# Kernel optimization log

Measured on AMD Instinct MI355X. Metric: run time of the kernel, lower is better.

Reference implementation:

```python
import math
import jax, jax.numpy as jnp
import numpy as np

NUM_HEAD = 16

def get_slopes(n):
    def pow2(n):
        start = 2 ** (-(2 ** (-(math.log2(n) - 3))))
        return [start * start ** i for i in range(n)]
    if math.log2(n).is_integer():
        return pow2(n)
    c = 2 ** math.floor(math.log2(n))
    return pow2(c) + get_slopes(2 * c)[0::2][: n - c]

def setup_inputs() -> dict:
    key = jax.random.key(0)
    ks = jax.random.split(key, 5)
    B, T, D = 2, 2048, 1024
    x = jax.random.normal(ks[0], (B, T, D), dtype=jnp.float32)
    Wq = jax.random.normal(ks[1], (D, D), dtype=jnp.float32) * 0.02
    Wk = jax.random.normal(ks[2], (D, D), dtype=jnp.float32) * 0.02
    Wv = jax.random.normal(ks[3], (D, D), dtype=jnp.float32) * 0.02
    Wo = jax.random.normal(ks[4], (D, D), dtype=jnp.float32) * (0.02 / math.sqrt(2 * 24))
    return {"x": x, "Wq": Wq, "Wk": Wk, "Wv": Wv, "Wo": Wo}

def reference(x, Wq, Wk, Wv, Wo):
    B, T, D = x.shape
    H = NUM_HEAD
    hd = D // H
    # projections (no bias)
    q = (x @ Wq).reshape(B, T, H, hd).transpose(0, 2, 1, 3)  # b h t d
    k = (x @ Wk).reshape(B, T, H, hd).transpose(0, 2, 1, 3)
    v = (x @ Wv).reshape(B, T, H, hd).transpose(0, 2, 1, 3)
    scores = jnp.einsum("bhqd,bhkd->bhqk", q, k) / jnp.sqrt(jnp.asarray(hd, dtype=q.dtype))
    # ALiBi bias: slopes[h] * (j - (T-1)), broadcast over query positions
    slopes = jnp.asarray(np.array(get_slopes(H), dtype=np.float32))
    alibi = slopes[:, None, None] * (jnp.arange(T, dtype=jnp.float32) - (T - 1))[None, None, :]  # h 1 k
    scores = scores + alibi[None]  # b h q k
    causal = jnp.tril(jnp.ones((T, T), dtype=bool))
    masked = jnp.where(causal[None, None], scores.astype(jnp.float32), jnp.finfo(jnp.float32).min)
    p = jax.nn.softmax(masked, axis=-1)
    attn_out = jnp.einsum("bhqk,bhkd->bhqd", p, v)
    attn_out = attn_out.transpose(0, 2, 1, 3).reshape(B, T, D)
    return attn_out @ Wo
```

## Files before the change

kernel.cpp:

```cpp
#include <hip/hip_runtime.h>
#include <hip/hip_bf16.h>
#include <math.h>

#define B_ 2
#define T_ 2048
#define D_ 1024
#define H_ 16
#define HD 64

typedef __bf16 bf16;
typedef bf16 bf16x8 __attribute__((ext_vector_type(8)));
typedef bf16 bf16x4 __attribute__((ext_vector_type(4)));
typedef short short4v __attribute__((ext_vector_type(4)));
typedef float f32x4 __attribute__((ext_vector_type(4)));

#define GL2LDS16(g, l) __builtin_amdgcn_global_load_lds(                      \
    (const __attribute__((address_space(1))) void*)(g),                       \
    (__attribute__((address_space(3))) void*)(l), 16, 0, 0)

static __device__ __forceinline__ f32x4 mfma16x16x16(bf16x4 a, bf16x4 b, f32x4 c) {
#if defined(__HIP_DEVICE_COMPILE__)
# if __has_builtin(__builtin_amdgcn_mfma_f32_16x16x16bf16_1k)
    return __builtin_amdgcn_mfma_f32_16x16x16bf16_1k(
        __builtin_bit_cast(short4v, a), __builtin_bit_cast(short4v, b), c, 0, 0, 0);
# else
    asm("v_mfma_f32_16x16x16_bf16 %0, %1, %2, %0" : "+v"(c) : "v"(a), "v"(b));
    return c;
# endif
#else
    (void)a; (void)b;
    return c;
#endif
}

static __device__ __forceinline__ bf16x4 lo4(bf16x8 v) {
    return __builtin_shufflevector(v, v, 0, 1, 2, 3);
}
static __device__ __forceinline__ bf16x4 hi4(bf16x8 v) {
    return __builtin_shufflevector(v, v, 4, 5, 6, 7);
}

__global__ __launch_bounds__(256) void prep_inputs(const float* __restrict__ x,
                                                   const float* __restrict__ W0,
                                                   const float* __restrict__ W1,
                                                   const float* __restrict__ W2,
                                                   const float* __restrict__ W3,
                                                   bf16* __restrict__ xb,
                                                   bf16* __restrict__ Wt) {
    const int z = blockIdx.z;
    const int tid = threadIdx.x;
    if (z >= 4) {
        size_t i = ((((size_t)(z - 4) * 256 + blockIdx.y * 16 + blockIdx.x) * 256) + tid) * 4;
        float4 v = *(const float4*)(x + i);
        bf16 tmp[4] = {(bf16)v.x, (bf16)v.y, (bf16)v.z, (bf16)v.w};
        *(uint2*)(xb + i) = *(const uint2*)tmp;
        return;
    }
    __shared__ bf16 tile[64 * 72];
    const float* W = (z == 0) ? W0 : (z == 1) ? W1 : (z == 2) ? W2 : W3;
    bf16* out = Wt + (size_t)z * D_ * D_;
    const int k0 = blockIdx.y * 64, n0 = blockIdx.x * 64;
    for (int it = 0; it < 4; ++it) {
        int idx = it * 256 + tid;
        int r = idx >> 4;
        int c4 = (idx & 15) << 2;
        float4 v = *(const float4*)(W + (size_t)(k0 + r) * D_ + n0 + c4);
        tile[(c4 + 0) * 72 + r] = (bf16)v.x;
        tile[(c4 + 1) * 72 + r] = (bf16)v.y;
        tile[(c4 + 2) * 72 + r] = (bf16)v.z;
        tile[(c4 + 3) * 72 + r] = (bf16)v.w;
    }
    __syncthreads();
    for (int it = 0; it < 2; ++it) {
        int idx = it * 256 + tid;
        int r = idx >> 3;
        int c8 = (idx & 7) << 3;
        bf16x8 v = *(const bf16x8*)&tile[r * 72 + c8];
        *(bf16x8*)(out + (size_t)(n0 + r) * D_ + k0 + c8) = v;
    }
}

__global__ __launch_bounds__(256) void gemm_qkv(const bf16* __restrict__ A,
                                                const bf16* __restrict__ Bt,
                                                bf16* __restrict__ Cout) {
    __shared__ bf16 As[2][128 * 32];
    __shared__ bf16 Bs[2][64 * 32];
    const int bid = blockIdx.x;
    const int xcd = bid & 7, rr = bid >> 3;
    const int y   = (xcd << 2) + (rr & 3);
    const int rem = rr >> 2;
    const int xx  = rem & 15;
    const int z   = rem >> 4;
    const int m0 = y * 128, n0 = xx * 64;

    const int tid = threadIdx.x;
    const int wave = tid >> 6, lane = tid & 63;
    const int quad = lane >> 4, l16 = lane & 15;
    const int wr = wave >> 1, wc = wave & 1;
    const bf16* Bz = Bt + (size_t)z * D_ * D_;

    const int lrow = lane >> 2, lcol = (lane & 3) << 3;
    const bf16* ag = A  + (size_t)(m0 + wave * 32 + lrow) * D_ + lcol;
    const bf16* bg = Bz + (size_t)(n0 + wave * 16 + lrow) * D_ + lcol;
    const int a_off = (wave * 32 + lrow) * 32 + lcol;
    const int b_off = (wave * 16 + lrow) * 32 + lcol;

    f32x4 acc[4][2];
    for (int mi = 0; mi < 4; ++mi)
        for (int ni = 0; ni < 2; ++ni) acc[mi][ni] = (f32x4){0.f, 0.f, 0.f, 0.f};

    for (int kb = 0; kb < D_; kb += 64) {
        GL2LDS16(ag + kb,                        &As[0][a_off]);
        GL2LDS16(ag + (size_t)16 * D_ + kb,      &As[0][a_off + 16 * 32]);
        GL2LDS16(ag + kb + 32,                   &As[1][a_off]);
        GL2LDS16(ag + (size_t)16 * D_ + kb + 32, &As[1][a_off + 16 * 32]);
        GL2LDS16(bg + kb,                        &Bs[0][b_off]);
        GL2LDS16(bg + kb + 32,                   &Bs[1][b_off]);
        __syncthreads();

        for (int half = 0; half < 2; ++half) {
            bf16x8 af[4], bfr[2];
            for (int mi = 0; mi < 4; ++mi)
                af[mi] = *(const bf16x8*)&As[half][(wr * 64 + mi * 16 + l16) * 32 + quad * 8];
            for (int ni = 0; ni < 2; ++ni)
                bfr[ni] = *(const bf16x8*)&Bs[half][(wc * 32 + ni * 16 + l16) * 32 + quad * 8];
            if (z < 2) {
                for (int mi = 0; mi < 4; ++mi)
                    for (int ni = 0; ni < 2; ++ni)
                        acc[mi][ni] = __builtin_amdgcn_mfma_f32_16x16x32_bf16(
                            bfr[ni], af[mi], acc[mi][ni], 0, 0, 0);
            } else {
                for (int mi = 0; mi < 4; ++mi)
                    for (int ni = 0; ni < 2; ++ni)
                        acc[mi][ni] = __builtin_amdgcn_mfma_f32_16x16x32_bf16(
                            af[mi], bfr[ni], acc[mi][ni], 0, 0, 0);
            }
        }
        __syncthreads();
    }

    bf16* Cb = Cout + (size_t)z * (B_ * T_) * D_;
    const float qscale = (z == 0) ? 0.180336887f : 1.0f;
    if (z < 2) {
        for (int mi = 0; mi < 4; ++mi)
            for (int ni = 0; ni < 2; ++ni) {
                int m = m0 + wr * 64 + mi * 16 + l16;
                int n = n0 + wc * 32 + ni * 16 + quad * 4;
                int b = m >> 11, t = m & (T_ - 1);
                int h = n >> 6, d = n & (HD - 1);
                bf16 o4[4];
                for (int r = 0; r < 4; ++r) o4[r] = (bf16)(acc[mi][ni][r] * qscale);
                *(uint2*)&Cb[(((((size_t)b * H_ + h) * T_ + t) << 6) + d)] =
                    *(const uint2*)o4;
            }
    } else {
        for (int mi = 0; mi < 4; ++mi)
            for (int ni = 0; ni < 2; ++ni) {
                int m = m0 + wr * 64 + mi * 16 + quad * 4;
                int n = n0 + wc * 32 + ni * 16 + l16;
                int b = m >> 11, t = m & (T_ - 1);
                int h = n >> 6, d = n & (HD - 1);
                bf16 o4[4];
                for (int r = 0; r < 4; ++r) o4[r] = (bf16)acc[mi][ni][r];
                *(uint2*)&Cb[((((size_t)b * H_ + h) * HD + d) * T_ + t)] =
                    *(const uint2*)o4;
            }
    }
}

__global__ __launch_bounds__(256) void gemm_out(const bf16* __restrict__ A,
                                                const bf16* __restrict__ Bt,
                                                float* __restrict__ Cout) {
    __shared__ bf16 As[2][128 * 32];
    __shared__ bf16 Bs[2][64 * 32];
    const int bid = blockIdx.x;
    const int xcd = bid & 7, rr = bid >> 3;
    const int y   = (xcd << 2) + (rr & 3);
    const int xx  = rr >> 2;
    const int m0 = y * 128, n0 = xx * 64;

    const int tid = threadIdx.x;
    const int wave = tid >> 6, lane = tid & 63;
    const int quad = lane >> 4, l16 = lane & 15;
    const int wr = wave >> 1, wc = wave & 1;

    const int lrow = lane >> 2, lcol = (lane & 3) << 3;
    const bf16* ag = A  + (size_t)(m0 + wave * 32 + lrow) * D_ + lcol;
    const bf16* bg = Bt + (size_t)(n0 + wave * 16 + lrow) * D_ + lcol;
    const int a_off = (wave * 32 + lrow) * 32 + lcol;
    const int b_off = (wave * 16 + lrow) * 32 + lcol;

    f32x4 acc[4][2];
    for (int mi = 0; mi < 4; ++mi)
        for (int ni = 0; ni < 2; ++ni) acc[mi][ni] = (f32x4){0.f, 0.f, 0.f, 0.f};

    for (int kb = 0; kb < D_; kb += 64) {
        GL2LDS16(ag + kb,                        &As[0][a_off]);
        GL2LDS16(ag + (size_t)16 * D_ + kb,      &As[0][a_off + 16 * 32]);
        GL2LDS16(ag + kb + 32,                   &As[1][a_off]);
        GL2LDS16(ag + (size_t)16 * D_ + kb + 32, &As[1][a_off + 16 * 32]);
        GL2LDS16(bg + kb,                        &Bs[0][b_off]);
        GL2LDS16(bg + kb + 32,                   &Bs[1][b_off]);
        __syncthreads();

        for (int half = 0; half < 2; ++half) {
            bf16x8 af[4], bfr[2];
            for (int mi = 0; mi < 4; ++mi)
                af[mi] = *(const bf16x8*)&As[half][(wr * 64 + mi * 16 + l16) * 32 + quad * 8];
            for (int ni = 0; ni < 2; ++ni)
                bfr[ni] = *(const bf16x8*)&Bs[half][(wc * 32 + ni * 16 + l16) * 32 + quad * 8];
            for (int mi = 0; mi < 4; ++mi)
                for (int ni = 0; ni < 2; ++ni)
                    acc[mi][ni] = __builtin_amdgcn_mfma_f32_16x16x32_bf16(
                        bfr[ni], af[mi], acc[mi][ni], 0, 0, 0);
        }
        __syncthreads();
    }

    for (int mi = 0; mi < 4; ++mi)
        for (int ni = 0; ni < 2; ++ni) {
            int m = m0 + wr * 64 + mi * 16 + l16;
            int n = n0 + wc * 32 + ni * 16 + quad * 4;
            *(f32x4*)&Cout[(size_t)m * D_ + n] = acc[mi][ni];
        }
}

__device__ __constant__ unsigned char ITEM_QT[24] = {
    8,9,10,11,12,13,14,15, 7,15, 6,14, 5,13, 4,12, 3,11, 2,10, 1,9, 0,8};
__device__ __constant__ unsigned char ITEM_KIND[24] = {
    1,1,1,1,1,1,1,1, 0,2, 0,2, 0,2, 0,2, 0,2, 0,2, 0,2, 0,2};

#define LDK 72
#define LDP 136

struct KVStage { bf16x8 k0, k1, v0, v1; };

__global__ __launch_bounds__(512, 4) void attn_kernel(const bf16* __restrict__ Q,
                                                      const bf16* __restrict__ K,
                                                      const bf16* __restrict__ Vt,
                                                      bf16* __restrict__ O,
                                                      float* __restrict__ Opart,
                                                      float2* __restrict__ ML) {
    __shared__ bf16 Ks[128 * LDK];
    __shared__ bf16 Vs[64 * LDP];

    const int bh = blockIdx.x;
    const int item = blockIdx.y;
    const int qt = ITEM_QT[item];
    const int kind = ITEM_KIND[item];
    const int h = bh & (H_ - 1), b = bh >> 4;
    const int tid = threadIdx.x;
    const int wave = tid >> 6, lane = tid & 63;
    const int quad = lane >> 4, l16 = lane & 15;

    const bf16* Qb = Q + (size_t)bh * T_ * HD;
    const bf16* Kb = K + (size_t)bh * T_ * HD;
    const bf16* Vb = Vt + (size_t)bh * HD * T_;

    const float slope2 = exp2f(-0.5f * (float)(h + 1)) * 1.44269504f;

    bf16x8 qf[2];
    {
        const bf16* qrow = Qb + (size_t)(qt * 128 + wave * 16 + l16) * HD + quad * 8;
        qf[0] = *(const bf16x8*)(qrow);
        qf[1] = *(const bf16x8*)(qrow + 32);
    }

    const int slot0 = tid, slot1 = 512 + tid;
    const int rk0 = slot0 >> 3, ck0 = (slot0 & 7) << 3;
    const int rk1 = slot1 >> 3, ck1 = (slot1 & 7) << 3;
    const int rv0 = slot0 >> 4, c0 = slot0 & 15;
    const int rv1 = slot1 >> 4, c1 = slot1 & 15;
    const int vs0 = rv0 * LDP + (c0 & 1) * 64 + (c0 >> 1) * 4;
    const int vs1 = rv1 * LDP + (c1 & 1) * 64 + (c1 >> 1) * 4;

    auto loadKV = [&](int t, KVStage& st) {
        const bf16* kb = Kb + (size_t)t * 128 * HD;
        st.k0 = *(const bf16x8*)(kb + rk0 * HD + ck0);
        st.k1 = *(const bf16x8*)(kb + rk1 * HD + ck1);
        const bf16* vb = Vb + t * 128;
        st.v0 = *(const bf16x8*)(vb + (size_t)rv0 * T_ + c0 * 8);
        st.v1 = *(const bf16x8*)(vb + (size_t)rv1 * T_ + c1 * 8);
    };
    auto storeKV = [&](const KVStage& st) {
        *(bf16x8*)&Ks[rk0 * LDK + ck0] = st.k0;
        *(bf16x8*)&Ks[rk1 * LDK + ck1] = st.k1;
        *(bf16x4*)&Vs[vs0]      = lo4(st.v0);
        *(bf16x4*)&Vs[vs0 + 32] = hi4(st.v0);
        *(bf16x4*)&Vs[vs1]      = lo4(st.v1);
        *(bf16x4*)&Vs[vs1 + 32] = hi4(st.v1);
    };

    f32x4 acc[4];
    for (int df = 0; df < 4; ++df) acc[df] = (f32x4){0.f, 0.f, 0.f, 0.f};
    float m_run = -INFINITY, l_lane = 0.f;

    const int qglob = qt * 128 + wave * 16 + l16;
    const int nkt = qt + 1;
    const int kt0 = (kind == 2) ? 8 : 0;
    const int kt1 = (kind == 1) ? 8 : nkt;

    auto compute = [&](int kt, bool last) {
        f32x4 s[8];
#pragma unroll
        for (int nf = 0; nf < 8; ++nf) {
            bf16x8 kf0 = *(const bf16x8*)&Ks[(nf * 16 + l16) * LDK + quad * 8];
            bf16x8 kf1 = *(const bf16x8*)&Ks[(nf * 16 + l16) * LDK + 32 + quad * 8];
            f32x4 zz = (f32x4){0.f, 0.f, 0.f, 0.f};
            __builtin_amdgcn_s_setprio(1);
            zz = __builtin_amdgcn_mfma_f32_16x16x32_bf16(kf0, qf[0], zz, 0, 0, 0);
            zz = __builtin_amdgcn_mfma_f32_16x16x32_bf16(kf1, qf[1], zz, 0, 0, 0);
            __builtin_amdgcn_s_setprio(0);
            s[nf] = zz;
        }

        const float j0f = (float)(kt * 128 + quad * 4 - (T_ - 1));
#pragma unroll
        for (int nf = 0; nf < 8; ++nf)
#pragma unroll
            for (int r = 0; r < 4; ++r)
                s[nf][r] += slope2 * (j0f + (float)(nf * 16 + r));
        if (last) {
            const int jb = kt * 128 + quad * 4;
#pragma unroll
            for (int nf = 0; nf < 8; ++nf)
#pragma unroll
                for (int r = 0; r < 4; ++r)
                    if (jb + nf * 16 + r > qglob) s[nf][r] = -INFINITY;
        }

        float a[8];
#pragma unroll
        for (int nf = 0; nf < 8; ++nf)
            a[nf] = fmaxf(fmaxf(s[nf][0], s[nf][1]), fmaxf(s[nf][2], s[nf][3]));
        float t0 = fmaxf(a[0], a[1]), t1 = fmaxf(a[2], a[3]);
        float t2 = fmaxf(a[4], a[5]), t3 = fmaxf(a[6], a[7]);
        float mx = fmaxf(fmaxf(t0, t1), fmaxf(t2, t3));
        mx = fmaxf(mx, __shfl_xor(mx, 16, 64));
        mx = fmaxf(mx, __shfl_xor(mx, 32, 64));

        if (!__all(mx - m_run <= 8.f)) {
            const float mnew = fmaxf(m_run, mx);
            const float alpha = exp2f(m_run - mnew);
            l_lane *= alpha;
#pragma unroll
            for (int df = 0; df < 4; ++df) acc[df] *= alpha;
            m_run = mnew;
        }

        float rs0 = 0.f, rs1 = 0.f;
        bf16x4 pf[8];
#pragma unroll
        for (int nf = 0; nf < 8; ++nf) {
            float p0 = exp2f(s[nf][0] - m_run);
            float p1 = exp2f(s[nf][1] - m_run);
            float p2 = exp2f(s[nf][2] - m_run);
            float p3 = exp2f(s[nf][3] - m_run);
            if (nf & 1) rs1 += (p0 + p1) + (p2 + p3);
            else        rs0 += (p0 + p1) + (p2 + p3);
            pf[nf] = (bf16x4){(bf16)p0, (bf16)p1, (bf16)p2, (bf16)p3};
        }
        l_lane += rs0 + rs1;

#pragma unroll
        for (int j = 0; j < 4; ++j) {
            bf16x8 w[4];
#pragma unroll
            for (int df = 0; df < 4; ++df)
                w[df] = *(const bf16x8*)&Vs[(df * 16 + l16) * LDP + quad * 32 + j * 8];
            __builtin_amdgcn_s_setprio(1);
#pragma unroll
            for (int df = 0; df < 4; ++df) {
                acc[df] = mfma16x16x16(lo4(w[df]), pf[2 * j],     acc[df]);
                acc[df] = mfma16x16x16(hi4(w[df]), pf[2 * j + 1], acc[df]);
            }
            __builtin_amdgcn_s_setprio(0);
        }
    };

    KVStage sA, sB;
    loadKV(kt0, sA);
    int kt = kt0;
    for (;;) {
        __syncthreads();
        storeKV(sA);
        if (kt + 1 < kt1) loadKV(kt + 1, sB);
        __syncthreads();
        compute(kt, kt == nkt - 1);
        if (++kt >= kt1) break;
        __syncthreads();
        storeKV(sB);
        if (kt + 1 < kt1) loadKV(kt + 1, sA);
        __syncthreads();
        compute(kt, kt == nkt - 1);
        if (++kt >= kt1) break;
    }

    float l_run = l_lane;
    l_run += __shfl_xor(l_run, 16, 64);
    l_run += __shfl_xor(l_run, 32, 64);

    if (kind == 0) {
        const float inv = 1.0f / l_run;
        for (int df = 0; df < 4; ++df) {
            bf16 o4[4];
            for (int r = 0; r < 4; ++r) o4[r] = (bf16)(acc[df][r] * inv);
            *(uint2*)&O[(((size_t)b * T_ + qglob) * H_ + h) * HD + df * 16 + quad * 4] =
                *(const uint2*)o4;
        }
    } else {
        const int pidx = (bh * 8 + (qt - 8)) * 2 + (kind == 2 ? 1 : 0);
        const int ql = wave * 16 + l16;
        float* dst = Opart + (size_t)pidx * 8192 + ql * 64;
        for (int df = 0; df < 4; ++df)
            *(f32x4*)&dst[df * 16 + quad * 4] = acc[df];
        if (quad == 0) ML[pidx * 128 + ql] = make_float2(m_run, l_run);
    }
}

__global__ __launch_bounds__(512) void attn_merge(const float* __restrict__ Opart,
                                                  const float2* __restrict__ ML,
                                                  bf16* __restrict__ O) {
    const int qt = 8 + blockIdx.x, bh = blockIdx.y;
    const int h = bh & (H_ - 1), b = bh >> 4;
    const int tid = threadIdx.x;
    const int q = tid >> 2, dc = (tid & 3) << 4;
    const int p0 = (bh * 8 + blockIdx.x) * 2, p1 = p0 + 1;

    const float2 ml0 = ML[p0 * 128 + q], ml1 = ML[p1 * 128 + q];
    const float M = fmaxf(ml0.x, ml1.x);
    const float e0 = exp2f(ml0.x - M), e1 = exp2f(ml1.x - M);
    const float inv = 1.0f / (e0 * ml0.y + e1 * ml1.y);

    const float* a = Opart + (size_t)p0 * 8192 + q * 64 + dc;
    const float* c = Opart + (size_t)p1 * 8192 + q * 64 + dc;
    bf16 o16[16];
    for (int j = 0; j < 4; ++j) {
        f32x4 va = *(const f32x4*)(a + j * 4);
        f32x4 vc = *(const f32x4*)(c + j * 4);
        for (int r = 0; r < 4; ++r)
            o16[j * 4 + r] = (bf16)((va[r] * e0 + vc[r] * e1) * inv);
    }
    const int t = qt * 128 + q;
    bf16* dst = O + (((size_t)b * T_ + t) * H_ + h) * HD + dc;
    *(bf16x8*)dst = *(const bf16x8*)o16;
    *(bf16x8*)(dst + 8) = *(const bf16x8*)(o16 + 8);
}

extern "C" void kernel_launch(void* const* d_in, const int* in_sizes, int n_in,
                              void* d_out, int out_size, void* d_ws, size_t ws_size,
                              hipStream_t stream) {
    const float* x  = (const float*)d_in[0];
    const float* Wq = (const float*)d_in[1];
    const float* Wk = (const float*)d_in[2];
    const float* Wv = (const float*)d_in[3];
    const float* Wo = (const float*)d_in[4];
    float* out = (float*)d_out;

    const size_t M = (size_t)B_ * T_;
    const size_t XE = M * D_;
    const size_t WE = (size_t)D_ * D_;

    char* ws = (char*)d_ws;
    size_t off = 0;
    auto carve = [&](size_t bytes) {
        void* p = ws + off;
        off += (bytes + 255) & ~(size_t)255;
        return p;
    };
    bf16* xb  = (bf16*)carve(XE * 2);
    bf16* Wt  = (bf16*)carve(4 * WE * 2);
    bf16* QKV = (bf16*)carve(3 * XE * 2);
    float*  Opart = (float*)carve(32 * 8 * 2 * 8192 * sizeof(float));
    float2* MLbuf = (float2*)carve(32 * 8 * 2 * 128 * sizeof(float2));
    bf16* attn = xb;

    prep_inputs<<<dim3(16, 16, 20), 256, 0, stream>>>(x, Wq, Wk, Wv, Wo, xb, Wt);

    gemm_qkv<<<1536, 256, 0, stream>>>(xb, Wt, QKV);
    attn_kernel<<<dim3(32, 24), 512, 0, stream>>>(QKV, QKV + XE, QKV + 2 * XE,
                                                  attn, Opart, MLbuf);
    attn_merge<<<dim3(8, 32), 512, 0, stream>>>(Opart, MLbuf, attn);
    gemm_out<<<512, 256, 0, stream>>>(attn, Wt + 3 * WE, out);
}
```

Before: 196.0 us.

## Compute Q, K and V tiles in one block to reuse the A tile

The QKV projection GEMM now has each block compute all three outputs (Q, K, V) for its 128x64 tile, with three accumulator sets, instead of launching a separate block per projection. The shared x tile is loaded into LDS once and reused across the three weight matrices, cutting global/LDS traffic for A by a factor of three. The grid shrinks from 1536 to 512 blocks, and accumulator registers and LDS for B triple, which may lower occupancy and reduce latency hiding.

```diff
diff --git a/kernel.cpp b/kernel.cpp
--- a/kernel.cpp
+++ b/kernel.cpp
@@ -84,87 +84,110 @@
                                                 const bf16* __restrict__ Bt,
                                                 bf16* __restrict__ Cout) {
     __shared__ bf16 As[2][128 * 32];
-    __shared__ bf16 Bs[2][64 * 32];
+    __shared__ bf16 Bs[3][2][64 * 32];
     const int bid = blockIdx.x;
     const int xcd = bid & 7, rr = bid >> 3;
     const int y   = (xcd << 2) + (rr & 3);
-    const int rem = rr >> 2;
-    const int xx  = rem & 15;
-    const int z   = rem >> 4;
+    const int xx  = rr >> 2;
     const int m0 = y * 128, n0 = xx * 64;
 
     const int tid = threadIdx.x;
     const int wave = tid >> 6, lane = tid & 63;
     const int quad = lane >> 4, l16 = lane & 15;
     const int wr = wave >> 1, wc = wave & 1;
-    const bf16* Bz = Bt + (size_t)z * D_ * D_;
 
     const int lrow = lane >> 2, lcol = (lane & 3) << 3;
-    const bf16* ag = A  + (size_t)(m0 + wave * 32 + lrow) * D_ + lcol;
-    const bf16* bg = Bz + (size_t)(n0 + wave * 16 + lrow) * D_ + lcol;
+    const bf16* ag = A + (size_t)(m0 + wave * 32 + lrow) * D_ + lcol;
+    const size_t brow = (size_t)(n0 + wave * 16 + lrow) * D_ + lcol;
     const int a_off = (wave * 32 + lrow) * 32 + lcol;
     const int b_off = (wave * 16 + lrow) * 32 + lcol;
 
-    f32x4 acc[4][2];
-    for (int mi = 0; mi < 4; ++mi)
-        for (int ni = 0; ni < 2; ++ni) acc[mi][ni] = (f32x4){0.f, 0.f, 0.f, 0.f};
+    f32x4 acc[3][4][2];
+#pragma unroll
+    for (int z = 0; z < 3; ++z)
+#pragma unroll
+        for (int mi = 0; mi < 4; ++mi)
+#pragma unroll
+            for (int ni = 0; ni < 2; ++ni) acc[z][mi][ni] = (f32x4){0.f, 0.f, 0.f, 0.f};
 
     for (int kb = 0; kb < D_; kb += 64) {
         GL2LDS16(ag + kb,                        &As[0][a_off]);
         GL2LDS16(ag + (size_t)16 * D_ + kb,      &As[0][a_off + 16 * 32]);
         GL2LDS16(ag + kb + 32,                   &As[1][a_off]);
         GL2LDS16(ag + (size_t)16 * D_ + kb + 32, &As[1][a_off + 16 * 32]);
-        GL2LDS16(bg + kb,                        &Bs[0][b_off]);
-        GL2LDS16(bg + kb + 32,                   &Bs[1][b_off]);
-        __syncthreads();
-
+#pragma unroll
+        for (int z = 0; z < 3; ++z) {
+            const bf16* bg = Bt + (size_t)z * D_ * D_ + brow;
+            GL2LDS16(bg + kb,      &Bs[z][0][b_off]);
+            GL2LDS16(bg + kb + 32, &Bs[z][1][b_off]);
+        }
+        __syncthreads();
+
+#pragma unroll
         for (int half = 0; half < 2; ++half) {
-            bf16x8 af[4], bfr[2];
+            bf16x8 af[4];
+#pragma unroll
             for (int mi = 0; mi < 4; ++mi)
                 af[mi] = *(const bf16x8*)&As[half][(wr * 64 + mi * 16 + l16) * 32 + quad * 8];
-            for (int ni = 0; ni < 2; ++ni)
-                bfr[ni] = *(const bf16x8*)&Bs[half][(wc * 32 + ni * 16 + l16) * 32 + quad * 8];
-            if (z < 2) {
-                for (int mi = 0; mi < 4; ++mi)
-                    for (int ni = 0; ni < 2; ++ni)
-                        acc[mi][ni] = __builtin_amdgcn_mfma_f32_16x16x32_bf16(
-                            bfr[ni], af[mi], acc[mi][ni], 0, 0, 0);
-            } else {
-                for (int mi = 0; mi < 4; ++mi)
-                    for (int ni = 0; ni < 2; ++ni)
-                        acc[mi][ni] = __builtin_amdgcn_mfma_f32_16x16x32_bf16(
-                            af[mi], bfr[ni], acc[mi][ni], 0, 0, 0);
+#pragma unroll
+            for (int z = 0; z < 3; ++z) {
+                bf16x8 bfr[2];
+#pragma unroll
+                for (int ni = 0; ni < 2; ++ni)
+                    bfr[ni] = *(const bf16x8*)&Bs[z][half][(wc * 32 + ni * 16 + l16) * 32 + quad * 8];
+                if (z < 2) {
+#pragma unroll
+                    for (int mi = 0; mi < 4; ++mi)
+#pragma unroll
+                        for (int ni = 0; ni < 2; ++ni)
+                            acc[z][mi][ni] = __builtin_amdgcn_mfma_f32_16x16x32_bf16(
+                                bfr[ni], af[mi], acc[z][mi][ni], 0, 0, 0);
+                } else {
+#pragma unroll
+                    for (int mi = 0; mi < 4; ++mi)
+#pragma unroll
+                        for (int ni = 0; ni < 2; ++ni)
+                            acc[z][mi][ni] = __builtin_amdgcn_mfma_f32_16x16x32_bf16(
+                                af[mi], bfr[ni], acc[z][mi][ni], 0, 0, 0);
+                }
             }
         }
         __syncthreads();
     }
 
-    bf16* Cb = Cout + (size_t)z * (B_ * T_) * D_;
-    const float qscale = (z == 0) ? 0.180336887f : 1.0f;
-    if (z < 2) {
-        for (int mi = 0; mi < 4; ++mi)
-            for (int ni = 0; ni < 2; ++ni) {
-                int m = m0 + wr * 64 + mi * 16 + l16;
-                int n = n0 + wc * 32 + ni * 16 + quad * 4;
-                int b = m >> 11, t = m & (T_ - 1);
-                int h = n >> 6, d = n & (HD - 1);
-                bf16 o4[4];
-                for (int r = 0; r < 4; ++r) o4[r] = (bf16)(acc[mi][ni][r] * qscale);
-                *(uint2*)&Cb[(((((size_t)b * H_ + h) * T_ + t) << 6) + d)] =
-                    *(const uint2*)o4;
-            }
-    } else {
-        for (int mi = 0; mi < 4; ++mi)
-            for (int ni = 0; ni < 2; ++ni) {
-                int m = m0 + wr * 64 + mi * 16 + quad * 4;
-                int n = n0 + wc * 32 + ni * 16 + l16;
-                int b = m >> 11, t = m & (T_ - 1);
-                int h = n >> 6, d = n & (HD - 1);
-                bf16 o4[4];
-                for (int r = 0; r < 4; ++r) o4[r] = (bf16)acc[mi][ni][r];
-                *(uint2*)&Cb[((((size_t)b * H_ + h) * HD + d) * T_ + t)] =
-                    *(const uint2*)o4;
-            }
+#pragma unroll
+    for (int z = 0; z < 3; ++z) {
+        bf16* Cb = Cout + (size_t)z * (B_ * T_) * D_;
+        const float qscale = (z == 0) ? 0.180336887f : 1.0f;
+        if (z < 2) {
+#pragma unroll
+            for (int mi = 0; mi < 4; ++mi)
+#pragma unroll
+                for (int ni = 0; ni < 2; ++ni) {
+                    int m = m0 + wr * 64 + mi * 16 + l16;
+                    int n = n0 + wc * 32 + ni * 16 + quad * 4;
+                    int b = m >> 11, t = m & (T_ - 1);
+                    int h = n >> 6, d = n & (HD - 1);
+                    bf16 o4[4];
+                    for (int r = 0; r < 4; ++r) o4[r] = (bf16)(acc[z][mi][ni][r] * qscale);
+                    *(uint2*)&Cb[(((((size_t)b * H_ + h) * T_ + t) << 6) + d)] =
+                        *(const uint2*)o4;
+                }
+        } else {
+#pragma unroll
+            for (int mi = 0; mi < 4; ++mi)
+#pragma unroll
+                for (int ni = 0; ni < 2; ++ni) {
+                    int m = m0 + wr * 64 + mi * 16 + quad * 4;
+                    int n = n0 + wc * 32 + ni * 16 + l16;
+                    int b = m >> 11, t = m & (T_ - 1);
+                    int h = n >> 6, d = n & (HD - 1);
+                    bf16 o4[4];
+                    for (int r = 0; r < 4; ++r) o4[r] = (bf16)acc[z][mi][ni][r];
+                    *(uint2*)&Cb[((((size_t)b * H_ + h) * HD + d) * T_ + t)] =
+                        *(const uint2*)o4;
+                }
+        }
     }
 }
 
@@ -477,7 +500,7 @@
 
     prep_inputs<<<dim3(16, 16, 20), 256, 0, stream>>>(x, Wq, Wk, Wv, Wo, xb, Wt);
 
-    gemm_qkv<<<1536, 256, 0, stream>>>(xb, Wt, QKV);
+    gemm_qkv<<<512, 256, 0, stream>>>(xb, Wt, QKV);
     attn_kernel<<<dim3(32, 24), 512, 0, stream>>>(QKV, QKV + XE, QKV + 2 * XE,
                                                   attn, Opart, MLbuf);
     attn_merge<<<dim3(8, 32), 512, 0, stream>>>(Opart, MLbuf, attn);
```

Result: faster. 189.4 us (-3.4%).
